# Optimization experiments

Hardware: AMD Instinct MI355X
Metric: run time of the kernel (lower is better)

Reference implementation:

```python
import jax, jax.numpy as jnp
import numpy as np

B, S, HID = 2, 4096, 640
NH, NKV, HD = 4, 1, 256
SCALING = 256.0 ** -0.5
SOFTCAP = 50.0
WINDOW = 512
EPS = 1e-6
ROPE_THETA = 10000.0  # local (sliding) rope base in Gemma3


def _rope_tables(seq_len, dim, theta):
    inv_freq = 1.0 / (theta ** (np.arange(0, dim, 2, dtype=np.float32) / dim))  # [dim/2]
    t = np.arange(seq_len, dtype=np.float32)
    freqs = np.outer(t, inv_freq)                      # [S, dim/2]
    emb = np.concatenate([freqs, freqs], axis=-1)      # [S, dim]
    return np.cos(emb)[None], np.sin(emb)[None]        # [1, S, dim]


def _sliding_causal_mask(b, s, window):
    i = np.arange(s)[:, None]
    j = np.arange(s)[None, :]
    allowed = (j <= i) & (j > i - window)              # causal + sliding window
    mask = np.where(allowed, 0.0, -1e9).astype(np.float32)
    return np.broadcast_to(mask[None, None], (b, 1, s, s)).copy()


def setup_inputs() -> dict:
    key = jax.random.key(0)
    ks = jax.random.split(key, 8)
    cos_np, sin_np = _rope_tables(S, HD, ROPE_THETA)
    return {
        "hidden_states": jax.random.normal(ks[0], (B, S, HID), jnp.float32),
        "cos": jnp.asarray(cos_np),
        "sin": jnp.asarray(sin_np),
        "attention_mask": jnp.asarray(_sliding_causal_mask(B, S, WINDOW)),
        "Wq": jax.random.normal(ks[1], (HID, NH * HD), jnp.float32) * 0.02,
        "Wk": jax.random.normal(ks[2], (HID, NKV * HD), jnp.float32) * 0.02,
        "Wv": jax.random.normal(ks[3], (HID, NKV * HD), jnp.float32) * 0.02,
        "Wo": jax.random.normal(ks[4], (NH * HD, HID), jnp.float32) * 0.02,
        "q_norm_w": jax.random.normal(ks[5], (HD,), jnp.float32) * 0.02,
        "k_norm_w": jax.random.normal(ks[6], (HD,), jnp.float32) * 0.02,
    }


def _rms_norm(x, w):
    var = jnp.mean(jnp.square(x), axis=-1, keepdims=True)
    return x * jax.lax.rsqrt(var + EPS) * (1.0 + w)


def _rotate_half(x):
    x1, x2 = jnp.split(x, 2, axis=-1)
    return jnp.concatenate([-x2, x1], axis=-1)


def _apply_rope(x, cos, sin):
    # x: [B, H, S, D]; cos/sin: [1, S, D] -> unsqueeze head dim
    c = cos[:, None, :, :]
    s = sin[:, None, :, :]
    return x * c + _rotate_half(x) * s


def reference(hidden_states, cos, sin, attention_mask, Wq, Wk, Wv, Wo, q_norm_w, k_norm_w):
    b, s, _ = hidden_states.shape
    # projections (no bias)
    q = (hidden_states @ Wq).reshape(b, s, NH, HD).transpose(0, 2, 1, 3)   # [B,NH,S,D]
    k = (hidden_states @ Wk).reshape(b, s, NKV, HD).transpose(0, 2, 1, 3)  # [B,1,S,D]
    v = (hidden_states @ Wv).reshape(b, s, NKV, HD).transpose(0, 2, 1, 3)  # [B,1,S,D]
    # per-head RMSNorm on q/k
    q = _rms_norm(q, q_norm_w)
    k = _rms_norm(k, k_norm_w)
    # RoPE
    q = _apply_rope(q, cos, sin)
    k = _apply_rope(k, cos, sin)
    # GQA: single kv head broadcast to all query heads
    k2 = k[:, 0]  # [B,S,D]
    v2 = v[:, 0]  # [B,S,D]
    scores = jnp.einsum('bhqd,bkd->bhqk', q, k2) * SCALING
    scores = SOFTCAP * jnp.tanh(scores / SOFTCAP)          # logit softcapping
    scores = scores + attention_mask                        # causal + sliding window
    attn = jax.nn.softmax(scores, axis=-1)
    out = jnp.einsum('bhqk,bkd->bhqd', attn, v2)            # [B,NH,S,D]
    out = out.transpose(0, 2, 1, 3).reshape(b, s, NH * HD)  # [B,S,NH*D]
    return out @ Wo                                         # [B,S,HID]
```

## Files before the change

kernel.cpp:

```cpp
#include <hip/hip_runtime.h>

typedef unsigned short u16;
typedef unsigned int u32;

typedef __attribute__((ext_vector_type(8)))  short bf16x8;
typedef __attribute__((ext_vector_type(4)))  float f32x4;

__device__ __forceinline__ float b2f(u16 u) {
    union { unsigned int i; float f; } v; v.i = ((unsigned int)u) << 16; return v.f;
}
__device__ __forceinline__ u16 f2b(float f) {
    union { float ff; unsigned int i; } v; v.ff = f;
    unsigned int x = v.i;
    return (u16)((x + 0x7fffu + ((x >> 16) & 1u)) >> 16);
}
__device__ __forceinline__ bool detect_bf16(const void* cosT) {
    return ((*(const u32*)cosT) & 0xffffu) == 0x3f80u;
}
__device__ __forceinline__ float4 ld4(const void* p, size_t off, bool isbf) {
    if (isbf) {
        ushort4 v = *(const ushort4*)((const u16*)p + off);
        return make_float4(b2f(v.x), b2f(v.y), b2f(v.z), b2f(v.w));
    }
    return *(const float4*)((const float*)p + off);
}
__device__ __forceinline__ float lds1(const void* p, size_t off, bool isbf) {
    return isbf ? b2f(((const u16*)p)[off]) : ((const float*)p)[off];
}
__device__ __forceinline__ void gll16(const void* g, void* l) {
    __builtin_amdgcn_global_load_lds(
        (const __attribute__((address_space(1))) u32*)g,
        (__attribute__((address_space(3))) u32*)l, 16, 0, 0);
}
__device__ __forceinline__ float capmask(float sdot, int i, int j) {
    float v = sdot * (0.0625f / 50.0f);
    v = fminf(fmaxf(v, -10.0f), 10.0f);
    float e = __expf(2.0f * v);
    float c = 50.0f * (e - 1.0f) / (e + 1.0f);
    bool allowed = (j <= i) && (j > i - 512);
    return allowed ? c : -1e30f;
}

__global__ __launch_bounds__(256) void prep(
    const void* __restrict__ hidden,
    const void* __restrict__ Wq, const void* __restrict__ Wk,
    const void* __restrict__ Wv, const void* __restrict__ Wo,
    const void* __restrict__ cosT,
    u16* __restrict__ Hb, u16* __restrict__ WT, u16* __restrict__ WoT)
{
    const bool isbf = detect_bf16(cosT);
    __shared__ float T[32][33];
    int id = blockIdx.x;
    if (id < 2560) {
        size_t base = ((size_t)id * 256 + threadIdx.x) * 8;
        if (isbf) {
            *(uint4*)(Hb + base) = *(const uint4*)((const u16*)hidden + base);
        } else {
            float4 a = ld4(hidden, base, false);
            float4 b = ld4(hidden, base + 4, false);
            uint4 o;
            o.x = (u32)f2b(a.x) | ((u32)f2b(a.y) << 16);
            o.y = (u32)f2b(a.z) | ((u32)f2b(a.w) << 16);
            o.z = (u32)f2b(b.x) | ((u32)f2b(b.y) << 16);
            o.w = (u32)f2b(b.z) | ((u32)f2b(b.w) << 16);
            *(uint4*)(Hb + base) = o;
        }
        return;
    }
    id -= 2560;
    const int tx = threadIdx.x & 31, ty = threadIdx.x >> 5;
    if (id < 960) {
        const int n0 = (id % 48) * 32, k0 = (id / 48) * 32;
        const void* src; int ldw, nof;
        if (n0 < 1024)      { src = Wq; ldw = 1024; nof = n0; }
        else if (n0 < 1280) { src = Wk; ldw = 256;  nof = n0 - 1024; }
        else                { src = Wv; ldw = 256;  nof = n0 - 1280; }
#pragma unroll
        for (int j = 0; j < 4; j++)
            T[ty + 8 * j][tx] = lds1(src, (size_t)(k0 + ty + 8 * j) * ldw + nof + tx, isbf);
        __syncthreads();
#pragma unroll
        for (int j = 0; j < 4; j++)
            WT[(size_t)(n0 + ty + 8 * j) * 640 + k0 + tx] = f2b(T[tx][ty + 8 * j]);
    } else {
        id -= 960;
        const int k0 = (id & 31) * 32, n0 = (id >> 5) * 32;
#pragma unroll
        for (int j = 0; j < 4; j++)
            T[ty + 8 * j][tx] = lds1(Wo, (size_t)(k0 + ty + 8 * j) * 640 + n0 + tx, isbf);
        __syncthreads();
#pragma unroll
        for (int j = 0; j < 4; j++)
            WoT[(size_t)(n0 + ty + 8 * j) * 1024 + k0 + tx] = f2b(T[tx][ty + 8 * j]);
    }
}

__global__ __launch_bounds__(256) void qkv_gemm(
    const u16* __restrict__ Hb, const u16* __restrict__ WT,
    u16* __restrict__ Qb, u16* __restrict__ Kb, u16* __restrict__ Vtg)
{
    const int n0 = blockIdx.x * 128, m0 = blockIdx.y * 128;
    const int t = threadIdx.x, w = t >> 6, lane = t & 63;
    const int l15 = lane & 15, quad = lane >> 4;
    const int wm = (w & 1) * 64, wn = (w >> 1) * 64;

    __shared__ __align__(16) u16 Ah[128][32];
    __shared__ __align__(16) u16 Bh[128][32];
    __shared__ __align__(16) u16 Sc[128][132];

    f32x4 acc[4][4];
#pragma unroll
    for (int i = 0; i < 4; i++)
#pragma unroll
        for (int j = 0; j < 4; j++) acc[i][j] = (f32x4)0.0f;

    for (int kb = 0; kb < 640; kb += 32) {
        __syncthreads();
#pragma unroll
        for (int i = 0; i < 2; i++) {
            int ci = t + 256 * i, m = ci >> 2, c = ci & 3;
            gll16(Hb + (size_t)(m0 + m) * 640 + kb + c * 8, (char*)&Ah[0][0] + ci * 16);
            gll16(WT + (size_t)(n0 + m) * 640 + kb + c * 8, (char*)&Bh[0][0] + ci * 16);
        }
        __syncthreads();
        bf16x8 af[4], bfr[4];
#pragma unroll
        for (int mi = 0; mi < 4; mi++)
            af[mi] = *(const bf16x8*)&Ah[wm + mi * 16 + l15][quad * 8];
#pragma unroll
        for (int ni = 0; ni < 4; ni++)
            bfr[ni] = *(const bf16x8*)&Bh[wn + ni * 16 + l15][quad * 8];
#pragma unroll
        for (int mi = 0; mi < 4; mi++)
#pragma unroll
            for (int ni = 0; ni < 4; ni++)
                acc[mi][ni] = __builtin_amdgcn_mfma_f32_16x16x32_bf16(
                    af[mi], bfr[ni], acc[mi][ni], 0, 0, 0);
    }

    if (n0 >= 1280) {
        const int bb = m0 >> 12, sblk = m0 & 4095;
#pragma unroll
        for (int mi = 0; mi < 4; mi++)
#pragma unroll
            for (int ni = 0; ni < 4; ni++) {
                int vd = n0 + wn + ni * 16 + l15 - 1280;
                int sb = sblk + wm + mi * 16 + quad * 4;
                ushort4 vv = make_ushort4(f2b(acc[mi][ni][0]), f2b(acc[mi][ni][1]),
                                          f2b(acc[mi][ni][2]), f2b(acc[mi][ni][3]));
                *(ushort4*)(Vtg + (size_t)bb * 1048576 + (size_t)vd * 4096 + sb) = vv;
            }
        return;
    }

    __syncthreads();
#pragma unroll
    for (int mi = 0; mi < 4; mi++)
#pragma unroll
        for (int ni = 0; ni < 4; ni++)
#pragma unroll
            for (int r = 0; r < 4; r++)
                Sc[wm + mi * 16 + quad * 4 + r][wn + ni * 16 + l15] = f2b(acc[mi][ni][r]);
    __syncthreads();

    u16* dst; int ldo, coff;
    if (n0 < 1024) { dst = Qb; ldo = 1024; coff = n0; }
    else           { dst = Kb; ldo = 256;  coff = n0 - 1024; }
#pragma unroll
    for (int i = 0; i < 8; i++) {
        int idx = t + 256 * i, r = idx >> 4, c = idx & 15;
        *(uint4*)(dst + (size_t)(m0 + r) * ldo + coff + c * 8) = *(const uint4*)&Sc[r][c * 8];
    }
}

__global__ __launch_bounds__(320) void norm_rope(
    u16* __restrict__ Qb, u16* __restrict__ Kb,
    const void* __restrict__ cosT, const void* __restrict__ sinT,
    const void* __restrict__ qw, const void* __restrict__ kw)
{
    const bool isbf = detect_bf16(cosT);
    const int row = blockIdx.x, s = row & 4095;
    const int g = threadIdx.x >> 6, lane = threadIdx.x & 63, d0 = lane * 4;

    u16* p; const void* w;
    if (g < 4) { p = Qb + (size_t)row * 1024 + g * 256 + d0; w = qw; }
    else       { p = Kb + (size_t)row * 256 + d0;            w = kw; }

    ushort4 xv = *(const ushort4*)p;
    float x0 = b2f(xv.x), x1 = b2f(xv.y), x2 = b2f(xv.z), x3 = b2f(xv.w);
    float ssum = x0 * x0 + x1 * x1 + x2 * x2 + x3 * x3;
#pragma unroll
    for (int off = 32; off > 0; off >>= 1) ssum += __shfl_xor(ssum, off, 64);
    float rs = rsqrtf(ssum * (1.0f / 256.0f) + 1e-6f);

    float4 wv = ld4(w, d0, isbf);
    float n0 = x0 * rs * (1.0f + wv.x);
    float n1 = x1 * rs * (1.0f + wv.y);
    float n2 = x2 * rs * (1.0f + wv.z);
    float n3 = x3 * rs * (1.0f + wv.w);

    float o0 = __shfl_xor(n0, 32, 64);
    float o1 = __shfl_xor(n1, 32, 64);
    float o2 = __shfl_xor(n2, 32, 64);
    float o3 = __shfl_xor(n3, 32, 64);
    float sgn = (lane < 32) ? -1.0f : 1.0f;

    float4 cv = ld4(cosT, (size_t)s * 256 + d0, isbf);
    float4 sv = ld4(sinT, (size_t)s * 256 + d0, isbf);
    *(ushort4*)p = make_ushort4(
        f2b(n0 * cv.x + sgn * o0 * sv.x), f2b(n1 * cv.y + sgn * o1 * sv.y),
        f2b(n2 * cv.z + sgn * o2 * sv.z), f2b(n3 * cv.w + sgn * o3 * sv.w));
}

__global__ __launch_bounds__(256, 2) void attn_mfma(
    const u16* __restrict__ Qb, const u16* __restrict__ Kb,
    const u16* __restrict__ Vtg, u16* __restrict__ AO)
{
    const int bx = blockIdx.x;
    const int q0 = (((bx & 7) << 5) + (bx >> 3)) * 16;
    const int b  = blockIdx.y;
    const int t = threadIdx.x, h = t >> 6, lane = t & 63;
    const int l15 = lane & 15, quad = lane >> 4;

    __shared__ __align__(16) u16 Ks[32][264];
    __shared__ __align__(16) u16 Vt[256][40];
    __shared__ __align__(16) u16 Pr[4][16][40];
    __shared__ float l_s[4][16];

    bf16x8 qf[8];
    {
        const u16* qp = Qb + ((size_t)(b * 4096 + q0 + l15)) * 1024 + h * 256 + quad * 8;
#pragma unroll
        for (int s = 0; s < 8; s++) qf[s] = *(const bf16x8*)(qp + s * 32);
    }

    f32x4 o[16];
#pragma unroll
    for (int i = 0; i < 16; i++) o[i] = (f32x4)0.0f;
    float lp[4] = {0.f, 0.f, 0.f, 0.f};

    const int lo = q0 - 511;
    const int jb0 = lo > 0 ? (lo >> 5) << 5 : 0;
    const int jb1 = (q0 + 15) & ~31;

    const u16* kbase = Kb + (size_t)b * 4096 * 256;
    const u16* vbase = Vtg + (size_t)b * 1048576;

    for (int jb = jb0; jb <= jb1; jb += 32) {
        __syncthreads();
#pragma unroll
        for (int i = 0; i < 4; i++) {
            int ci = t + 256 * i;
            *(uint4*)&Ks[ci >> 5][(ci & 31) * 8] =
                *(const uint4*)(kbase + (size_t)(jb + (ci >> 5)) * 256 + (ci & 31) * 8);
            *(uint4*)&Vt[ci >> 2][(ci & 3) * 8] =
                *(const uint4*)(vbase + (size_t)(ci >> 2) * 4096 + jb + (ci & 3) * 8);
        }
        __syncthreads();

        f32x4 s0 = (f32x4)0.0f, s1 = (f32x4)0.0f;
#pragma unroll
        for (int ds = 0; ds < 8; ds++) {
            bf16x8 kf0 = *(const bf16x8*)&Ks[l15][ds * 32 + quad * 8];
            bf16x8 kf1 = *(const bf16x8*)&Ks[16 + l15][ds * 32 + quad * 8];
            s0 = __builtin_amdgcn_mfma_f32_16x16x32_bf16(qf[ds], kf0, s0, 0, 0, 0);
            s1 = __builtin_amdgcn_mfma_f32_16x16x32_bf16(qf[ds], kf1, s1, 0, 0, 0);
        }
        const int j0 = jb + l15;
#pragma unroll
        for (int r = 0; r < 4; r++) {
            int qi = q0 + quad * 4 + r;
            float p0 = __expf(capmask(s0[r], qi, j0));
            float p1 = __expf(capmask(s1[r], qi, j0 + 16));
            u16 pb0 = f2b(p0), pb1 = f2b(p1);
            Pr[h][quad * 4 + r][l15]      = pb0;
            Pr[h][quad * 4 + r][16 + l15] = pb1;
            lp[r] += b2f(pb0) + b2f(pb1);
        }
        __threadfence_block();
        bf16x8 pf = *(const bf16x8*)&Pr[h][l15][quad * 8];
#pragma unroll
        for (int mt = 0; mt < 16; mt++) {
            bf16x8 vf = *(const bf16x8*)&Vt[mt * 16 + l15][quad * 8];
            o[mt] = __builtin_amdgcn_mfma_f32_16x16x32_bf16(vf, pf, o[mt], 0, 0, 0);
        }
    }

#pragma unroll
    for (int r = 0; r < 4; r++) {
        float v = lp[r];
        v += __shfl_xor(v, 1, 64); v += __shfl_xor(v, 2, 64);
        v += __shfl_xor(v, 4, 64); v += __shfl_xor(v, 8, 64);
        lp[r] = v;
    }
    if (l15 == 0) {
#pragma unroll
        for (int r = 0; r < 4; r++) l_s[h][quad * 4 + r] = lp[r];
    }
    __threadfence_block();
    __syncthreads();
    const float inv = 1.0f / l_s[h][l15];

    u16* aop = AO + ((size_t)(b * 4096 + q0 + l15)) * 1024 + h * 256 + quad * 4;
#pragma unroll
    for (int mt = 0; mt < 16; mt++) {
        *(ushort4*)(aop + mt * 16) = make_ushort4(
            f2b(o[mt][0] * inv), f2b(o[mt][1] * inv),
            f2b(o[mt][2] * inv), f2b(o[mt][3] * inv));
    }
}

__global__ __launch_bounds__(256) void out_gemm(
    const u16* __restrict__ AO, const u16* __restrict__ WoT,
    const void* __restrict__ cosT, void* __restrict__ outp)
{
    const bool isbf = detect_bf16(cosT);
    const int n0 = blockIdx.x * 64, m0 = blockIdx.y * 128;
    const int t = threadIdx.x, w = t >> 6, lane = t & 63;
    const int l15 = lane & 15, quad = lane >> 4;
    const int wm = (w & 1) * 64, wn = (w >> 1) * 32;

    __shared__ __align__(16) u16 Ah[128][32];
    __shared__ __align__(16) u16 Bh[64][32];
    __shared__ __align__(16) float Scf[128][68];

    f32x4 acc[4][2];
#pragma unroll
    for (int i = 0; i < 4; i++)
#pragma unroll
        for (int j = 0; j < 2; j++) acc[i][j] = (f32x4)0.0f;

    for (int kb = 0; kb < 1024; kb += 32) {
        __syncthreads();
#pragma unroll
        for (int i = 0; i < 2; i++) {
            int ci = t + 256 * i, m = ci >> 2, c = ci & 3;
            gll16(AO + (size_t)(m0 + m) * 1024 + kb + c * 8, (char*)&Ah[0][0] + ci * 16);
        }
        {
            int m = t >> 2, c = t & 3;
            gll16(WoT + (size_t)(n0 + m) * 1024 + kb + c * 8, (char*)&Bh[0][0] + t * 16);
        }
        __syncthreads();
        bf16x8 af[4], bfr[2];
#pragma unroll
        for (int mi = 0; mi < 4; mi++)
            af[mi] = *(const bf16x8*)&Ah[wm + mi * 16 + l15][quad * 8];
#pragma unroll
        for (int ni = 0; ni < 2; ni++)
            bfr[ni] = *(const bf16x8*)&Bh[wn + ni * 16 + l15][quad * 8];
#pragma unroll
        for (int mi = 0; mi < 4; mi++)
#pragma unroll
            for (int ni = 0; ni < 2; ni++)
                acc[mi][ni] = __builtin_amdgcn_mfma_f32_16x16x32_bf16(
                    af[mi], bfr[ni], acc[mi][ni], 0, 0, 0);
    }

    __syncthreads();
#pragma unroll
    for (int mi = 0; mi < 4; mi++)
#pragma unroll
        for (int ni = 0; ni < 2; ni++)
#pragma unroll
            for (int r = 0; r < 4; r++)
                Scf[wm + mi * 16 + quad * 4 + r][wn + ni * 16 + l15] = acc[mi][ni][r];
    __syncthreads();

    if (isbf) {
#pragma unroll
        for (int i = 0; i < 4; i++) {
            int idx = t + 256 * i, r = idx >> 3, c = idx & 7;
            ushort4 lo4 = make_ushort4(
                f2b(Scf[r][c * 8 + 0]), f2b(Scf[r][c * 8 + 1]),
                f2b(Scf[r][c * 8 + 2]), f2b(Scf[r][c * 8 + 3]));
            ushort4 hi4 = make_ushort4(
                f2b(Scf[r][c * 8 + 4]), f2b(Scf[r][c * 8 + 5]),
                f2b(Scf[r][c * 8 + 6]), f2b(Scf[r][c * 8 + 7]));
            u16* p = (u16*)outp + (size_t)(m0 + r) * 640 + n0 + c * 8;
            *(ushort4*)p = lo4; *(ushort4*)(p + 4) = hi4;
        }
    } else {
#pragma unroll
        for (int i = 0; i < 8; i++) {
            int idx = t + 256 * i, r = idx >> 4, c = idx & 15;
            float4 v = *(const float4*)&Scf[r][c * 4];
            *(float4*)((float*)outp + (size_t)(m0 + r) * 640 + n0 + c * 4) = v;
        }
    }
}

extern "C" void kernel_launch(void* const* d_in, const int* in_sizes, int n_in,
                              void* d_out, int out_size, void* d_ws, size_t ws_size,
                              hipStream_t stream) {
    const void* hidden = d_in[0];
    const void* cosT   = d_in[1];
    const void* sinT   = d_in[2];
    const void* Wq     = d_in[4];
    const void* Wk     = d_in[5];
    const void* Wv     = d_in[6];
    const void* Wo     = d_in[7];
    const void* qw     = d_in[8];
    const void* kw     = d_in[9];

    char* ws = (char*)d_ws;
    u16* Hb  = (u16*)ws;
    u16* WT  = (u16*)(ws + 10485760);
    u16* AO  = (u16*)ws;
    u16* WoT = (u16*)(ws + 16777216);
    u16* Qb  = (u16*)(ws + 18087936);
    u16* Kb  = (u16*)(ws + 34865152);
    u16* Vtg = (u16*)(ws + 39059456);

    prep<<<dim3(4160), 256, 0, stream>>>(hidden, Wq, Wk, Wv, Wo, cosT, Hb, WT, WoT);
    qkv_gemm<<<dim3(12, 64), 256, 0, stream>>>(Hb, WT, Qb, Kb, Vtg);
    norm_rope<<<dim3(8192), 320, 0, stream>>>(Qb, Kb, cosT, sinT, qw, kw);
    attn_mfma<<<dim3(256, 2), 256, 0, stream>>>(Qb, Kb, Vtg, AO);
    out_gemm<<<dim3(10, 64), 256, 0, stream>>>(AO, WoT, cosT, d_out);
}
```

Baseline: 331.8 us.

## Split attention KV range across two blocks and deepen GEMM k-steps

The attention kernel now splits each query tile's key range into two halves handled by separate blocks. Each block writes an unnormalized bf16 partial output and its row sums, and a new combine kernel adds the partials and normalizes. This doubles the attention grid to improve CU occupancy, at the cost of an extra kernel launch and extra memory traffic for the partials. The QKV and output GEMMs also load 64-wide k chunks per barrier pair instead of 32, halving the number of syncs, and reuse one shared buffer for the staging and epilogue tiles. The split appears to rely on softmax without a running max, so partial sums add directly; partial outputs are rounded to bf16 before combining.

```diff
diff --git a/kernel.cpp b/kernel.cpp
--- a/kernel.cpp
+++ b/kernel.cpp
@@ -104,9 +104,9 @@
     const int l15 = lane & 15, quad = lane >> 4;
     const int wm = (w & 1) * 64, wn = (w >> 1) * 64;
 
-    __shared__ __align__(16) u16 Ah[128][32];
-    __shared__ __align__(16) u16 Bh[128][32];
-    __shared__ __align__(16) u16 Sc[128][132];
+    __shared__ __align__(16) char smem[33792];
+    u16* Ap = (u16*)smem;
+    u16* Bp = (u16*)(smem + 16384);
 
     f32x4 acc[4][4];
 #pragma unroll
@@ -114,28 +114,35 @@
 #pragma unroll
         for (int j = 0; j < 4; j++) acc[i][j] = (f32x4)0.0f;
 
-    for (int kb = 0; kb < 640; kb += 32) {
-        __syncthreads();
-#pragma unroll
-        for (int i = 0; i < 2; i++) {
-            int ci = t + 256 * i, m = ci >> 2, c = ci & 3;
-            gll16(Hb + (size_t)(m0 + m) * 640 + kb + c * 8, (char*)&Ah[0][0] + ci * 16);
-            gll16(WT + (size_t)(n0 + m) * 640 + kb + c * 8, (char*)&Bh[0][0] + ci * 16);
-        }
-        __syncthreads();
-        bf16x8 af[4], bfr[4];
-#pragma unroll
-        for (int mi = 0; mi < 4; mi++)
-            af[mi] = *(const bf16x8*)&Ah[wm + mi * 16 + l15][quad * 8];
-#pragma unroll
-        for (int ni = 0; ni < 4; ni++)
-            bfr[ni] = *(const bf16x8*)&Bh[wn + ni * 16 + l15][quad * 8];
-#pragma unroll
-        for (int mi = 0; mi < 4; mi++)
+    for (int kb = 0; kb < 640; kb += 64) {
+        __syncthreads();
+#pragma unroll
+        for (int p = 0; p < 2; p++)
+#pragma unroll
+            for (int i = 0; i < 2; i++) {
+                int ci = t + 256 * i, m = ci >> 2, c = ci & 3;
+                gll16(Hb + (size_t)(m0 + m) * 640 + kb + p * 32 + c * 8,
+                      smem + p * 8192 + ci * 16);
+                gll16(WT + (size_t)(n0 + m) * 640 + kb + p * 32 + c * 8,
+                      smem + 16384 + p * 8192 + ci * 16);
+            }
+        __syncthreads();
+#pragma unroll
+        for (int p = 0; p < 2; p++) {
+            bf16x8 af[4], bfr[4];
+#pragma unroll
+            for (int mi = 0; mi < 4; mi++)
+                af[mi] = *(const bf16x8*)&Ap[p * 4096 + (wm + mi * 16 + l15) * 32 + quad * 8];
 #pragma unroll
             for (int ni = 0; ni < 4; ni++)
-                acc[mi][ni] = __builtin_amdgcn_mfma_f32_16x16x32_bf16(
-                    af[mi], bfr[ni], acc[mi][ni], 0, 0, 0);
+                bfr[ni] = *(const bf16x8*)&Bp[p * 4096 + (wn + ni * 16 + l15) * 32 + quad * 8];
+#pragma unroll
+            for (int mi = 0; mi < 4; mi++)
+#pragma unroll
+                for (int ni = 0; ni < 4; ni++)
+                    acc[mi][ni] = __builtin_amdgcn_mfma_f32_16x16x32_bf16(
+                        af[mi], bfr[ni], acc[mi][ni], 0, 0, 0);
+        }
     }
 
     if (n0 >= 1280) {
@@ -154,6 +161,7 @@
     }
 
     __syncthreads();
+    u16 (*Sc)[132] = (u16(*)[132])smem;
 #pragma unroll
     for (int mi = 0; mi < 4; mi++)
 #pragma unroll
@@ -214,18 +222,17 @@
 
 __global__ __launch_bounds__(256, 2) void attn_mfma(
     const u16* __restrict__ Qb, const u16* __restrict__ Kb,
-    const u16* __restrict__ Vtg, u16* __restrict__ AO)
+    const u16* __restrict__ Vtg, u16* __restrict__ OAb, float* __restrict__ Lp)
 {
     const int bx = blockIdx.x;
     const int q0 = (((bx & 7) << 5) + (bx >> 3)) * 16;
-    const int b  = blockIdx.y;
+    const int b  = blockIdx.y & 1, split = blockIdx.y >> 1;
     const int t = threadIdx.x, h = t >> 6, lane = t & 63;
     const int l15 = lane & 15, quad = lane >> 4;
 
     __shared__ __align__(16) u16 Ks[32][264];
     __shared__ __align__(16) u16 Vt[256][40];
     __shared__ __align__(16) u16 Pr[4][16][40];
-    __shared__ float l_s[4][16];
 
     bf16x8 qf[8];
     {
@@ -242,11 +249,15 @@
     const int lo = q0 - 511;
     const int jb0 = lo > 0 ? (lo >> 5) << 5 : 0;
     const int jb1 = (q0 + 15) & ~31;
+    const int niters = ((jb1 - jb0) >> 5) + 1;
+    const int half0 = (niters + 1) >> 1;
+    const int my_lo = split ? jb0 + half0 * 32 : jb0;
+    const int my_hi = split ? jb1 : jb0 + (half0 - 1) * 32;
 
     const u16* kbase = Kb + (size_t)b * 4096 * 256;
     const u16* vbase = Vtg + (size_t)b * 1048576;
 
-    for (int jb = jb0; jb <= jb1; jb += 32) {
+    for (int jb = my_lo; jb <= my_hi; jb += 32) {
         __syncthreads();
 #pragma unroll
         for (int i = 0; i < 4; i++) {
@@ -295,19 +306,34 @@
     }
     if (l15 == 0) {
 #pragma unroll
-        for (int r = 0; r < 4; r++) l_s[h][quad * 4 + r] = lp[r];
-    }
-    __threadfence_block();
-    __syncthreads();
-    const float inv = 1.0f / l_s[h][l15];
-
-    u16* aop = AO + ((size_t)(b * 4096 + q0 + l15)) * 1024 + h * 256 + quad * 4;
+        for (int r = 0; r < 4; r++)
+            Lp[((size_t)(split * 2 + b) * 4 + h) * 4096 + q0 + quad * 4 + r] = lp[r];
+    }
+
+    u16* oap = OAb + ((size_t)((split * 2 + b) * 4096 + q0 + l15)) * 1024 + h * 256 + quad * 4;
 #pragma unroll
     for (int mt = 0; mt < 16; mt++) {
-        *(ushort4*)(aop + mt * 16) = make_ushort4(
-            f2b(o[mt][0] * inv), f2b(o[mt][1] * inv),
-            f2b(o[mt][2] * inv), f2b(o[mt][3] * inv));
-    }
+        *(ushort4*)(oap + mt * 16) = make_ushort4(
+            f2b(o[mt][0]), f2b(o[mt][1]), f2b(o[mt][2]), f2b(o[mt][3]));
+    }
+}
+
+__global__ __launch_bounds__(256) void combine(
+    const u16* __restrict__ OAb, const float* __restrict__ Lp, u16* __restrict__ AO)
+{
+    const int row = blockIdx.x;
+    const int b = row >> 12, q = row & 4095;
+    const int t = threadIdx.x, h = t >> 6;
+    const float l0 = Lp[((size_t)(b) * 4 + h) * 4096 + q];
+    const float l1 = Lp[((size_t)(2 + b) * 4 + h) * 4096 + q];
+    const float inv = 1.0f / (l0 + l1);
+    const size_t i0 = ((size_t)b * 4096 + q) * 1024 + t * 4;
+    const size_t i1 = ((size_t)(2 + b) * 4096 + q) * 1024 + t * 4;
+    ushort4 a = *(const ushort4*)(OAb + i0);
+    ushort4 c = *(const ushort4*)(OAb + i1);
+    *(ushort4*)(AO + (size_t)row * 1024 + t * 4) = make_ushort4(
+        f2b((b2f(a.x) + b2f(c.x)) * inv), f2b((b2f(a.y) + b2f(c.y)) * inv),
+        f2b((b2f(a.z) + b2f(c.z)) * inv), f2b((b2f(a.w) + b2f(c.w)) * inv));
 }
 
 __global__ __launch_bounds__(256) void out_gemm(
@@ -320,9 +346,9 @@
     const int l15 = lane & 15, quad = lane >> 4;
     const int wm = (w & 1) * 64, wn = (w >> 1) * 32;
 
-    __shared__ __align__(16) u16 Ah[128][32];
-    __shared__ __align__(16) u16 Bh[64][32];
-    __shared__ __align__(16) float Scf[128][68];
+    __shared__ __align__(16) char smem[34816];
+    u16* Ap = (u16*)smem;
+    u16* Bp = (u16*)(smem + 16384);
 
     f32x4 acc[4][2];
 #pragma unroll
@@ -330,34 +356,43 @@
 #pragma unroll
         for (int j = 0; j < 2; j++) acc[i][j] = (f32x4)0.0f;
 
-    for (int kb = 0; kb < 1024; kb += 32) {
-        __syncthreads();
-#pragma unroll
-        for (int i = 0; i < 2; i++) {
-            int ci = t + 256 * i, m = ci >> 2, c = ci & 3;
-            gll16(AO + (size_t)(m0 + m) * 1024 + kb + c * 8, (char*)&Ah[0][0] + ci * 16);
-        }
-        {
-            int m = t >> 2, c = t & 3;
-            gll16(WoT + (size_t)(n0 + m) * 1024 + kb + c * 8, (char*)&Bh[0][0] + t * 16);
-        }
-        __syncthreads();
-        bf16x8 af[4], bfr[2];
-#pragma unroll
-        for (int mi = 0; mi < 4; mi++)
-            af[mi] = *(const bf16x8*)&Ah[wm + mi * 16 + l15][quad * 8];
-#pragma unroll
-        for (int ni = 0; ni < 2; ni++)
-            bfr[ni] = *(const bf16x8*)&Bh[wn + ni * 16 + l15][quad * 8];
-#pragma unroll
-        for (int mi = 0; mi < 4; mi++)
+    for (int kb = 0; kb < 1024; kb += 64) {
+        __syncthreads();
+#pragma unroll
+        for (int p = 0; p < 2; p++) {
+#pragma unroll
+            for (int i = 0; i < 2; i++) {
+                int ci = t + 256 * i, m = ci >> 2, c = ci & 3;
+                gll16(AO + (size_t)(m0 + m) * 1024 + kb + p * 32 + c * 8,
+                      smem + p * 8192 + ci * 16);
+            }
+            {
+                int m = t >> 2, c = t & 3;
+                gll16(WoT + (size_t)(n0 + m) * 1024 + kb + p * 32 + c * 8,
+                      smem + 16384 + p * 4096 + t * 16);
+            }
+        }
+        __syncthreads();
+#pragma unroll
+        for (int p = 0; p < 2; p++) {
+            bf16x8 af[4], bfr[2];
+#pragma unroll
+            for (int mi = 0; mi < 4; mi++)
+                af[mi] = *(const bf16x8*)&Ap[p * 4096 + (wm + mi * 16 + l15) * 32 + quad * 8];
 #pragma unroll
             for (int ni = 0; ni < 2; ni++)
-                acc[mi][ni] = __builtin_amdgcn_mfma_f32_16x16x32_bf16(
-                    af[mi], bfr[ni], acc[mi][ni], 0, 0, 0);
+                bfr[ni] = *(const bf16x8*)&Bp[p * 2048 + (wn + ni * 16 + l15) * 32 + quad * 8];
+#pragma unroll
+            for (int mi = 0; mi < 4; mi++)
+#pragma unroll
+                for (int ni = 0; ni < 2; ni++)
+                    acc[mi][ni] = __builtin_amdgcn_mfma_f32_16x16x32_bf16(
+                        af[mi], bfr[ni], acc[mi][ni], 0, 0, 0);
+        }
     }
 
     __syncthreads();
+    float (*Scf)[68] = (float(*)[68])smem;
 #pragma unroll
     for (int mi = 0; mi < 4; mi++)
 #pragma unroll
@@ -411,10 +446,13 @@
     u16* Qb  = (u16*)(ws + 18087936);
     u16* Kb  = (u16*)(ws + 34865152);
     u16* Vtg = (u16*)(ws + 39059456);
+    u16* OAb = (u16*)(ws + 43253760);
+    float* Lp = (float*)(ws + 76808192);
 
     prep<<<dim3(4160), 256, 0, stream>>>(hidden, Wq, Wk, Wv, Wo, cosT, Hb, WT, WoT);
     qkv_gemm<<<dim3(12, 64), 256, 0, stream>>>(Hb, WT, Qb, Kb, Vtg);
     norm_rope<<<dim3(8192), 320, 0, stream>>>(Qb, Kb, cosT, sinT, qw, kw);
-    attn_mfma<<<dim3(256, 2), 256, 0, stream>>>(Qb, Kb, Vtg, AO);
+    attn_mfma<<<dim3(256, 4), 256, 0, stream>>>(Qb, Kb, Vtg, OAb, Lp);
+    combine<<<dim3(8192), 256, 0, stream>>>(OAb, Lp, AO);
     out_gemm<<<dim3(10, 64), 256, 0, stream>>>(AO, WoT, cosT, d_out);
 }
```

Result: slower. 342.0 us (+3.1%).
